# Kernel optimization log

Hardware: AMD Instinct MI355X
Metric: run time of the kernel (lower is better)

Reference implementation:

```python
import jax, jax.numpy as jnp
import numpy as np
from jax import lax

T = 50
THETA = 1.0 - 0.0001  # max_1 - 0.0001, max_1 = T_win/T = 1.0


def conv_t(x, w, b, pad_h):
    # x: [N, C, H, W, T]; slayer conv3d has time-kernel 1 -> conv2d per timestep.
    n, c, h, wd, t = x.shape
    xb = jnp.moveaxis(x, -1, 1).reshape(n * t, c, h, wd)
    y = lax.conv_general_dilated(xb, w, (1, 1), [(pad_h, pad_h), (0, 0)])
    y = y + b[None, :, None, None]
    o, h2, w2 = y.shape[1], y.shape[2], y.shape[3]
    return jnp.moveaxis(y.reshape(n, t, o, h2, w2), 1, -1)


def if_spikes(a):
    # catCuda.getSpikes on an input stacked T times: IF neuron with constant
    # drive a per step, soft reset (v -= theta on spike). a: [N,C,H,W].
    def step(v, _):
        v = v + a
        s = (v >= THETA).astype(a.dtype)
        return v - s * THETA, s
    _, sp = lax.scan(step, jnp.zeros_like(a), None, length=T)
    return jnp.moveaxis(sp, 0, -1)  # [N,C,H,W,T]


def setup_inputs() -> dict:
    key = jax.random.key(0)
    ks = jax.random.split(key, 6)
    def w(k, shape, scale):
        return jax.random.normal(k, shape, jnp.float32) * scale
    x = jax.random.uniform(ks[0], (256, 1, 180, 1, T), jnp.float32)
    return {
        'x': x,
        'w1': w(ks[1], (16, 1, 3, 1), 0.3), 'b1': jnp.zeros(16, jnp.float32),
        'w2': w(ks[2], (32, 16, 9, 1), 0.1), 'b2': jnp.zeros(32, jnp.float32),
        'w3': w(ks[3], (32, 32, 7, 1), 0.1), 'b3': jnp.zeros(32, jnp.float32),
        'wf': w(ks[4], (4, 32, 83, 1), 0.05), 'bf': jnp.zeros(4, jnp.float32),
    }


def reference(x, w1, b1, w2, b2, w3, b3, wf, bf):
    y = conv_t(x, w1, b1, 1)                        # [N,16,180,1,T]
    y = if_spikes(jnp.sum(y, axis=4) / T)           # rate -> spikes
    y = conv_t(y, w2, b2, 1)                        # [N,32,174,1,T]
    y = if_spikes(jnp.sum(y, axis=4) / T)
    y = 1.1 * (y[:, :, 0::2] + y[:, :, 1::2])       # slayer sum-pool (2,1), weight 1.1
    y = if_spikes(jnp.sum(y, axis=4) / T)           # [N,32,87,1,T]
    y = conv_t(y, w3, b3, 1)                        # [N,32,83,1,T]
    y = if_spikes(jnp.sum(y, axis=4) / T)
    out = jnp.einsum('nchwt,ochw->not', y, wf) + bf[None, :, None]  # dense over full spatial
    return jnp.sum(out, axis=-1) / T                # sum_spikes / T -> [N,4]
```

## Files before the change

### kernel.cpp

```cpp
#include <hip/hip_runtime.h>


#define T_STEPS 50
#define THETA   0.9999f

template<int W>
__device__ __forceinline__ void spike_rate_w(const float* a, float* r) {
    float v[W], c[W];
#pragma unroll
    for (int w = 0; w < W; ++w) { v[w] = 0.f; c[w] = 0.f; }
#pragma unroll
    for (int k = 0; k < T_STEPS; ++k) {
#pragma unroll
        for (int w = 0; w < W; ++w) {
            v[w] += a[w];
            float s = (v[w] >= THETA) ? 1.0f : 0.0f;
            v[w] -= s * THETA;
            c[w] += s;
        }
    }
#pragma unroll
    for (int w = 0; w < W; ++w) r[w] = c[w] / 50.0f;
}

__device__ __forceinline__ float spike_rate1(float a) {
    float r;
    spike_rate_w<1>(&a, &r);
    return r;
}

extern "C" __global__ void __launch_bounds__(1024)
catnet_kernel(const float* __restrict__ x,
              const float* __restrict__ w1, const float* __restrict__ b1,
              const float* __restrict__ w2, const float* __restrict__ b2,
              const float* __restrict__ w3, const float* __restrict__ b3,
              const float* __restrict__ wf, const float* __restrict__ bf,
              float* __restrict__ out)
{
    const int n    = blockIdx.x;
    const int tid  = threadIdx.x;
    const int wave = tid >> 6;
    const int lane = tid & 63;

    __shared__ float xbar[182];
    __shared__ float r1p[16][182];
    __shared__ float r2s[32][174];
    __shared__ float r3p[32][89];
    __shared__ float r4s[32][83];
    __shared__ float part[16];

    if (tid < 16)              { r1p[tid][0] = 0.f; r1p[tid][181] = 0.f; }
    if (tid >= 32 && tid < 64) { r3p[tid-32][0] = 0.f; r3p[tid-32][88] = 0.f; }
    if (tid == 64)             { xbar[0] = 0.f; xbar[181] = 0.f; }

    const float* xn = x + (size_t)n * (180 * 50);
    if (tid < 720) {
        const int h = tid >> 2, q = tid & 3;
        const float* row = xn + h * 50;
        float s = 0.f;
        for (int t = q; t < T_STEPS; t += 4) s += row[t];
        s += __shfl_xor(s, 1, 4);
        s += __shfl_xor(s, 2, 4);
        if (q == 0) xbar[h + 1] = s;
    }
    __syncthreads();

    for (int idx = tid; idx < 16 * 180; idx += 1024) {
        int c = idx / 180, h = idx - c * 180;
        float a = w1[c*3+0] * xbar[h] + w1[c*3+1] * xbar[h+1] + w1[c*3+2] * xbar[h+2];
        a = a / 50.0f + b1[c];
        r1p[c][h + 1] = spike_rate1(a);
    }
    __syncthreads();

    {
        const int ucg   = __builtin_amdgcn_readfirstlane(wave >> 1);
        const int half  = wave & 1;
        const int hbase = half * 87;
        const int h0 = hbase + lane;
        const int h1 = hbase + 64 + lane;
        const bool v1 = lane < 23;
        const int h1r = v1 ? h1 : h0;
        const float* wb = w2 + ucg * 4 * 144;

        float a[8];
#pragma unroll
        for (int j = 0; j < 4; ++j) { a[j] = b2[ucg*4 + j]; a[4+j] = a[j]; }

        for (int ci = 0; ci < 16; ++ci) {
            float r0[9], r1v[9];
#pragma unroll
            for (int kh = 0; kh < 9; ++kh) {
                r0[kh]  = r1p[ci][h0 + kh];
                r1v[kh] = r1p[ci][h1r + kh];
            }
#pragma unroll
            for (int j = 0; j < 4; ++j) {
                const float* wj = wb + j * 144 + ci * 9;
#pragma unroll
                for (int kh = 0; kh < 9; ++kh) {
                    float wv = wj[kh];
                    a[j]   += wv * r0[kh];
                    a[4+j] += wv * r1v[kh];
                }
            }
        }
        float r[8];
        spike_rate_w<8>(a, r);
#pragma unroll
        for (int j = 0; j < 4; ++j) {
            r2s[ucg*4 + j][h0] = r[j];
            if (v1) r2s[ucg*4 + j][h1] = r[4+j];
        }
    }
    __syncthreads();

    for (int idx = tid; idx < 32 * 87; idx += 1024) {
        int c = idx / 87, h = idx - c * 87;
        float a = 1.1f * (r2s[c][2*h] + r2s[c][2*h + 1]);
        r3p[c][h + 1] = spike_rate1(a);
    }
    __syncthreads();

    {
        const int ucg   = __builtin_amdgcn_readfirstlane(wave >> 1);
        const int half  = wave & 1;
        const int hbase = half * 42;
        const int cnt   = half ? 41 : 42;
        const bool v0   = lane < cnt;
        const int h0    = hbase + (v0 ? lane : 0);
        const float* wb = w3 + ucg * 4 * 224;

        float a[4];
#pragma unroll
        for (int j = 0; j < 4; ++j) a[j] = b3[ucg*4 + j];

        for (int ci = 0; ci < 32; ++ci) {
            float rv[7];
#pragma unroll
            for (int kh = 0; kh < 7; ++kh) rv[kh] = r3p[ci][h0 + kh];
#pragma unroll
            for (int j = 0; j < 4; ++j) {
                const float* wj = wb + j * 224 + ci * 7;
#pragma unroll
                for (int kh = 0; kh < 7; ++kh)
                    a[j] += wj[kh] * rv[kh];
            }
        }
        float r[4];
        spike_rate_w<4>(a, r);
        if (v0) {
#pragma unroll
            for (int j = 0; j < 4; ++j) r4s[ucg*4 + j][h0] = r[j];
        }
    }
    __syncthreads();

    {
        const int o = wave >> 2, q = wave & 3;
        const float* r4f = &r4s[0][0];
        const float* wo  = wf + o * (32 * 83);
        float acc = 0.f;
        for (int j = q * 64 + lane; j < 32 * 83; j += 256)
            acc += r4f[j] * wo[j];
#pragma unroll
        for (int off = 32; off > 0; off >>= 1)
            acc += __shfl_down(acc, off, 64);
        if (lane == 0) part[wave] = acc;
    }
    __syncthreads();
    if (tid < 4) {
        float s = part[tid*4] + part[tid*4+1] + part[tid*4+2] + part[tid*4+3];
        out[n * 4 + tid] = s + bf[tid];
    }
}

extern "C" void kernel_launch(void* const* d_in, const int* in_sizes, int n_in,
                              void* d_out, int out_size, void* d_ws, size_t ws_size,
                              hipStream_t stream) {
    const float* x  = (const float*)d_in[0];
    const float* w1 = (const float*)d_in[1];
    const float* b1 = (const float*)d_in[2];
    const float* w2 = (const float*)d_in[3];
    const float* b2 = (const float*)d_in[4];
    const float* w3 = (const float*)d_in[5];
    const float* b3 = (const float*)d_in[6];
    const float* wf = (const float*)d_in[7];
    const float* bf = (const float*)d_in[8];
    float* outp = (float*)d_out;

    catnet_kernel<<<dim3(256), dim3(1024), 0, stream>>>(
        x, w1, b1, w2, b2, w3, b3, wf, bf, outp);
}
```

Measured before the change: 119.0 us.

## Replace 50-step IF spike simulation with closed-form floor count plus exact fallback

The spike count of an integrate-and-fire neuron with constant drive is computed in closed form as floor(50*a/theta), clamped to [0,50], instead of simulating 50 steps. When any lane in the wave has a value near an integer boundary, where float rounding could make the closed form disagree with the step-by-step result, the whole wave falls back to the exact sequential loop. This removes most of the serial ALU work in the four spike stages. In exchange it adds a wave-wide ballot branch whose fallback is a non-unrolled loop, and exactness depends on the tolerance chosen.

```diff
diff --git a/kernel.cpp b/kernel.cpp
--- a/kernel.cpp
+++ b/kernel.cpp
@@ -4,29 +4,23 @@
 #define T_STEPS 50
 #define THETA   0.9999f
 
-template<int W>
-__device__ __forceinline__ void spike_rate_w(const float* a, float* r) {
-    float v[W], c[W];
-#pragma unroll
-    for (int w = 0; w < W; ++w) { v[w] = 0.f; c[w] = 0.f; }
-#pragma unroll
-    for (int k = 0; k < T_STEPS; ++k) {
-#pragma unroll
-        for (int w = 0; w < W; ++w) {
-            v[w] += a[w];
-            float s = (v[w] >= THETA) ? 1.0f : 0.0f;
-            v[w] -= s * THETA;
-            c[w] += s;
+__device__ __forceinline__ float spike_rate(float a) {
+    constexpr float INV = 50.0f / 0.9999f;
+    float t = a * INV;
+    float c = fminf(fmaxf(floorf(t), 0.0f), 50.0f);
+    bool risky = (t > 0.5f) && (fabsf(t - rintf(t)) < 5e-4f);
+    if (__ballot(risky)) {
+        float v = 0.f, cnt = 0.f;
+#pragma unroll 1
+        for (int k = 0; k < T_STEPS; ++k) {
+            v += a;
+            float s = (v >= THETA) ? 1.0f : 0.0f;
+            v -= s * THETA;
+            cnt += s;
         }
+        c = cnt;
     }
-#pragma unroll
-    for (int w = 0; w < W; ++w) r[w] = c[w] / 50.0f;
-}
-
-__device__ __forceinline__ float spike_rate1(float a) {
-    float r;
-    spike_rate_w<1>(&a, &r);
-    return r;
+    return c / 50.0f;
 }
 
 extern "C" __global__ void __launch_bounds__(1024)
@@ -69,7 +63,7 @@
         int c = idx / 180, h = idx - c * 180;
         float a = w1[c*3+0] * xbar[h] + w1[c*3+1] * xbar[h+1] + w1[c*3+2] * xbar[h+2];
         a = a / 50.0f + b1[c];
-        r1p[c][h + 1] = spike_rate1(a);
+        r1p[c][h + 1] = spike_rate(a);
     }
     __syncthreads();
 
@@ -105,12 +99,11 @@
                 }
             }
         }
-        float r[8];
-        spike_rate_w<8>(a, r);
 #pragma unroll
         for (int j = 0; j < 4; ++j) {
-            r2s[ucg*4 + j][h0] = r[j];
-            if (v1) r2s[ucg*4 + j][h1] = r[4+j];
+            r2s[ucg*4 + j][h0] = spike_rate(a[j]);
+            float rj = spike_rate(a[4+j]);
+            if (v1) r2s[ucg*4 + j][h1] = rj;
         }
     }
     __syncthreads();
@@ -118,7 +111,7 @@
     for (int idx = tid; idx < 32 * 87; idx += 1024) {
         int c = idx / 87, h = idx - c * 87;
         float a = 1.1f * (r2s[c][2*h] + r2s[c][2*h + 1]);
-        r3p[c][h + 1] = spike_rate1(a);
+        r3p[c][h + 1] = spike_rate(a);
     }
     __syncthreads();
 
@@ -147,11 +140,10 @@
                     a[j] += wj[kh] * rv[kh];
             }
         }
-        float r[4];
-        spike_rate_w<4>(a, r);
-        if (v0) {
 #pragma unroll
-            for (int j = 0; j < 4; ++j) r4s[ucg*4 + j][h0] = r[j];
+        for (int j = 0; j < 4; ++j) {
+            float rj = spike_rate(a[j]);
+            if (v0) r4s[ucg*4 + j][h0] = rj;
         }
     }
     __syncthreads();
```

After: 105.9 us. -11.0%, faster.
